# Kernel optimization log

Measured on AMD Instinct MI355X. Metric: run time of the kernel, lower is better.

Reference implementation:

```python
import jax, jax.numpy as jnp
import numpy as np

B, S, D_IN, D_HID, D_OUT, H = 2, 2048, 1024, 1024, 1024, 16
HD = D_HID // H  # head_dim = 64


def setup_inputs() -> dict:
    key = jax.random.key(0)
    ks = jax.random.split(key, 9)
    s_in = 1.0 / np.sqrt(D_IN)
    s_out = 1.0 / np.sqrt(D_OUT)
    return {
        "x": jax.random.normal(ks[0], (B, S, D_IN), dtype=jnp.float32),
        "Wq": jax.random.uniform(ks[1], (D_IN, D_HID), jnp.float32, -s_in, s_in),
        "bq": jax.random.uniform(ks[2], (D_HID,), jnp.float32, -s_in, s_in),
        "Wk": jax.random.uniform(ks[3], (D_IN, D_HID), jnp.float32, -s_in, s_in),
        "bk": jax.random.uniform(ks[4], (D_HID,), jnp.float32, -s_in, s_in),
        "Wv": jax.random.uniform(ks[5], (D_IN, D_OUT), jnp.float32, -s_in, s_in),
        "bv": jax.random.uniform(ks[6], (D_OUT,), jnp.float32, -s_in, s_in),
        "Wo": jax.random.uniform(ks[7], (D_OUT, D_OUT), jnp.float32, -s_out, s_out),
        "bo": jax.random.uniform(ks[8], (D_OUT,), jnp.float32, -s_out, s_out),
    }


def reference(x, Wq, bq, Wk, bk, Wv, bv, Wo, bo):
    b, s, _ = x.shape
    q = (x @ Wq + bq).reshape(b, s, H, HD)  # [B,S,H,HD]
    k = (x @ Wk + bk).reshape(b, s, H, HD)
    v = (x @ Wv + bv).reshape(b, s, H, HD)
    scores = jnp.einsum("bqhd,bkhd->bhqk", q, k) / jnp.sqrt(jnp.float32(HD))
    attn = jax.nn.softmax(scores, axis=-1)  # [B,H,S,S]
    ctx = jnp.einsum("bhqk,bkhd->bqhd", attn, v).reshape(b, s, D_HID)
    return ctx @ Wo + bo
```

## Files before the change

kernel.cpp:

```cpp
#include <hip/hip_runtime.h>
#include <stdint.h>

typedef __attribute__((ext_vector_type(8))) short short8v;
typedef __attribute__((ext_vector_type(4))) short short4v;
typedef __attribute__((ext_vector_type(4))) float float4v;
typedef __attribute__((ext_vector_type(4))) unsigned short ushort4v;
typedef __attribute__((ext_vector_type(4))) float floatvec4;
typedef __attribute__((ext_vector_type(2))) unsigned int uint2v;

#define DEVI __device__ __forceinline__

DEVI unsigned short f2bf(float f) {
    unsigned int u = __builtin_bit_cast(unsigned int, f);
    u += 0x7FFFu + ((u >> 16) & 1u);
    return (unsigned short)(u >> 16);
}

DEVI unsigned int pk2bf(float a, float b) {
#if defined(__has_builtin) && __has_builtin(__builtin_amdgcn_cvt_pk_bf16_f32)
    auto r = __builtin_amdgcn_cvt_pk_bf16_f32(a, b);
    unsigned int u;
    __builtin_memcpy(&u, &r, 4);
    return u;
#else
    return (unsigned int)f2bf(a) | ((unsigned int)f2bf(b) << 16);
#endif
}

DEVI float ex2(float x) {
#if defined(__has_builtin) && __has_builtin(__builtin_amdgcn_exp2f)
    return __builtin_amdgcn_exp2f(x);
#else
    return __builtin_exp2f(x);
#endif
}

typedef __attribute__((address_space(1))) void GV;
typedef __attribute__((address_space(3))) void LV;
DEVI void gl2lds16(const void* g, void* l) {
    __builtin_amdgcn_global_load_lds((GV*)g, (LV*)l, 16, 0, 0);
}

__global__ void prep_kernel(const float* __restrict__ x, unsigned short* __restrict__ xb,
                            const float* __restrict__ W0, const float* __restrict__ W1,
                            const float* __restrict__ W2, const float* __restrict__ W3,
                            unsigned short* __restrict__ D0, unsigned short* __restrict__ D1,
                            unsigned short* __restrict__ D2, unsigned short* __restrict__ D3) {
    const int bid = blockIdx.x, tid = threadIdx.x;
    if (bid < 4096) {
        const int i = (bid * 256 + tid) * 4;
        const floatvec4 v = *(const floatvec4*)&x[i];
        ushort4v o;
#pragma unroll
        for (int r = 0; r < 4; r++) o[r] = f2bf(v[r]);
        *(ushort4v*)&xb[i] = o;
        return;
    }
    __shared__ float t[32][33];
    const int tcode = bid - 4096;
    const int z = tcode >> 10, rem = tcode & 1023;
    const int by = rem >> 5, bx = rem & 31;
    const int tx = tid & 31, ty = tid >> 5;
    const float* W = (z == 0) ? W0 : (z == 1) ? W1 : (z == 2) ? W2 : W3;
    unsigned short* D = (z == 0) ? D0 : (z == 1) ? D1 : (z == 2) ? D2 : D3;
#pragma unroll
    for (int i = 0; i < 4; i++)
        t[ty + i * 8][tx] = W[(size_t)(by * 32 + ty + i * 8) * 1024 + bx * 32 + tx];
    __syncthreads();
#pragma unroll
    for (int i = 0; i < 4; i++)
        D[(size_t)(bx * 32 + ty + i * 8) * 1024 + by * 32 + tx] = f2bf(t[tx][ty + i * 8]);
}

__global__ __launch_bounds__(256, 3) void qkv_gemm(
    const unsigned short* __restrict__ X, const unsigned short* __restrict__ Wt,
    const float* __restrict__ bq, const float* __restrict__ bk, const float* __restrict__ bv,
    unsigned short* __restrict__ qb, unsigned short* __restrict__ kb,
    unsigned short* __restrict__ vtb)
{
    __shared__ __align__(16) unsigned short As[128 * 64];
    __shared__ __align__(16) unsigned short Bs[128 * 64];
    const int tid = threadIdx.x, lane = tid & 63, wv = tid >> 6;
    const int quad = lane >> 4, l16 = lane & 15;
    const int w = blockIdx.x >> 3;
    const int n0 = (blockIdx.x & 7) * 128;
    const int row0 = blockIdx.y * 128;
    const unsigned short* Wsel = Wt + (size_t)w * (1024 * 1024);

    const int srow = lane >> 3;
    const int qsc = ((lane & 7) ^ (lane >> 3 & 7)) * 8;
    const int fsw = l16 & 7;
    const int wm = (wv >> 1) * 64, wn = (wv & 1) * 64;

    float4v acc[4][4];
#pragma unroll
    for (int i = 0; i < 4; i++)
#pragma unroll
        for (int j = 0; j < 4; j++) acc[i][j] = (float4v){0.f, 0.f, 0.f, 0.f};

    for (int k0 = 0; k0 < 1024; k0 += 64) {
        __syncthreads();
#pragma unroll
        for (int i = 0; i < 4; i++) {
            const int c = wv * 4 + i;
            gl2lds16(X + (size_t)(row0 + c * 8 + srow) * 1024 + k0 + qsc, As + c * 512);
            gl2lds16(Wsel + (size_t)(n0 + c * 8 + srow) * 1024 + k0 + qsc, Bs + c * 512);
        }
        __syncthreads();
#pragma unroll
        for (int kc = 0; kc < 2; kc++) {
            const int sl = (((kc * 4 + quad) ^ fsw) * 8);
            short8v a[4], b[4];
#pragma unroll
            for (int mt = 0; mt < 4; mt++)
                a[mt] = *(const short8v*)&As[(wm + mt * 16 + l16) * 64 + sl];
#pragma unroll
            for (int nt = 0; nt < 4; nt++)
                b[nt] = *(const short8v*)&Bs[(wn + nt * 16 + l16) * 64 + sl];
#pragma unroll
            for (int mt = 0; mt < 4; mt++)
#pragma unroll
                for (int nt = 0; nt < 4; nt++)
                    acc[mt][nt] = __builtin_amdgcn_mfma_f32_16x16x32_bf16(a[mt], b[nt], acc[mt][nt], 0, 0, 0);
        }
    }

    const float* bias = (w == 0) ? bq : (w == 1) ? bk : bv;
    const float scl = (w == 0) ? 0.18033688011112042f : 1.0f;
#pragma unroll
    for (int nt = 0; nt < 4; nt++) {
        const int col = n0 + wn + nt * 16 + l16;
        const float bb = bias[col];
        const int h = col >> 6, hd = col & 63;
#pragma unroll
        for (int mt = 0; mt < 4; mt++) {
            const int tok0 = row0 + wm + mt * 16 + quad * 4;
            const int b_ = tok0 >> 11, s0 = tok0 & 2047;
            if (w == 2) {
                ushort4v pk;
#pragma unroll
                for (int r = 0; r < 4; r++) pk[r] = f2bf(acc[mt][nt][r] + bb);
                *(ushort4v*)&vtb[(((size_t)b_ * 16 + h) * 64 + hd) * 2048 + s0] = pk;
            } else {
                unsigned short* dst = (w == 0) ? qb : kb;
#pragma unroll
                for (int r = 0; r < 4; r++)
                    dst[(((size_t)b_ * 16 + h) * 2048 + (s0 + r)) * 64 + hd] =
                        f2bf((acc[mt][nt][r] + bb) * scl);
            }
        }
    }
}

__global__ __launch_bounds__(256, 2) void attn_kernel(
    const unsigned short* __restrict__ qb, const unsigned short* __restrict__ kb,
    const unsigned short* __restrict__ vtb, unsigned short* __restrict__ ctxb)
{
    __shared__ __align__(16) unsigned short Kt[128 * 64];
    __shared__ __align__(16) unsigned short Vt[64 * 128];
    __shared__ __align__(16) unsigned short Pb[4][32 * 128];
    const int tid = threadIdx.x, lane = tid & 63, wv = tid >> 6;
    const int quad = lane >> 4, l16 = lane & 15;
    const int bh = blockIdx.x, qt = blockIdx.y;
    const size_t boff = (size_t)bh * (2048 * 64);
    const unsigned short* qp = qb + boff;
    const unsigned short* kp = kb + boff;
    const unsigned short* vp = vtb + boff;
    const int q0 = qt * 128 + wv * 32;

    short8v qf[2][2];
#pragma unroll
    for (int nt = 0; nt < 2; nt++)
#pragma unroll
        for (int kc = 0; kc < 2; kc++)
            qf[nt][kc] = *(const short8v*)&qp[(size_t)(q0 + nt * 16 + l16) * 64 + kc * 32 + quad * 8];

    float4v accO[2][4];
#pragma unroll
    for (int nt = 0; nt < 2; nt++)
#pragma unroll
        for (int ht = 0; ht < 4; ht++) accO[nt][ht] = (float4v){0.f, 0.f, 0.f, 0.f};
    float lsum[2] = {0.f, 0.f};

    const int krow = lane >> 3;
    const int kg = (lane & 7) ^ (lane >> 3);
    const int vrow = lane >> 4;
    const int rsw = l16 & 7;

    const int ktb0 = l16 * 64 + ((quad ^ rsw) * 8);
    const int ktb1 = l16 * 64 + (((4 + quad) ^ rsw) * 8);
    const int vrb = l16 * 128 + ((quad ^ (l16 & 3)) * 8);
    const int l12e = (l16 & 12) * 8;
    const int prow = l16 * 128;

    for (int kt0 = 0; kt0 < 2048; kt0 += 128) {
        __syncthreads();
#pragma unroll
        for (int i = 0; i < 4; i++) {
            const int c = wv * 4 + i;
            gl2lds16(kp + (size_t)(kt0 + c * 8 + krow) * 64 + kg * 8, Kt + c * 512);
            const int vr = c * 4 + vrow;
            const int vg = (lane & 15) ^ (vr & 15);
            gl2lds16(vp + (size_t)vr * 2048 + kt0 + vg * 8, Vt + c * 512);
        }
        __syncthreads();

#pragma unroll
        for (int mt = 0; mt < 8; mt++) {
            const short8v a0 = *(const short8v*)&Kt[ktb0 + mt * 1024];
            const short8v a1 = *(const short8v*)&Kt[ktb1 + mt * 1024];
            const int pwo = prow + (((mt * 4 + quad) ^ l16) * 4);
#pragma unroll
            for (int nt = 0; nt < 2; nt++) {
                float4v z = (float4v){0.f, 0.f, 0.f, 0.f};
                z = __builtin_amdgcn_mfma_f32_16x16x32_bf16(a0, qf[nt][0], z, 0, 0, 0);
                z = __builtin_amdgcn_mfma_f32_16x16x32_bf16(a1, qf[nt][1], z, 0, 0, 0);
                const float p0 = ex2(z[0]), p1 = ex2(z[1]);
                const float p2 = ex2(z[2]), p3 = ex2(z[3]);
                lsum[nt] += (p0 + p1) + (p2 + p3);
                *(uint2v*)&Pb[wv][pwo + nt * 2048] = (uint2v){pk2bf(p0, p1), pk2bf(p2, p3)};
            }
        }
        asm volatile("s_waitcnt lgkmcnt(0)" ::: "memory");

#pragma unroll
        for (int kc = 0; kc < 4; kc++) {
            const int roff = (kc * 32) ^ l12e;
            short8v bvv[4];
#pragma unroll
            for (int ht = 0; ht < 4; ht++)
                bvv[ht] = *(const short8v*)&Vt[vrb + roff + ht * 2048];
            const int c0 = prow + (((kc * 8 + quad * 2) ^ l16) * 4);
            const int c1 = prow + (((kc * 8 + quad * 2 + 1) ^ l16) * 4);
#pragma unroll
            for (int nt = 0; nt < 2; nt++) {
                const short4v d0 = *(const short4v*)&Pb[wv][c0 + nt * 2048];
                const short4v d1 = *(const short4v*)&Pb[wv][c1 + nt * 2048];
                const short8v ap = __builtin_shufflevector(d0, d1, 0, 1, 2, 3, 4, 5, 6, 7);
#pragma unroll
                for (int ht = 0; ht < 4; ht++)
                    accO[nt][ht] = __builtin_amdgcn_mfma_f32_16x16x32_bf16(ap, bvv[ht], accO[nt][ht], 0, 0, 0);
            }
        }
    }

#pragma unroll
    for (int nt = 0; nt < 2; nt++) {
        lsum[nt] += __shfl_xor(lsum[nt], 16);
        lsum[nt] += __shfl_xor(lsum[nt], 32);
    }

    const int b_ = bh >> 4, h = bh & 15;
#pragma unroll
    for (int nt = 0; nt < 2; nt++)
#pragma unroll
        for (int r = 0; r < 4; r++) {
            const int s = q0 + nt * 16 + quad * 4 + r;
            const float inv = 1.0f / __shfl(lsum[nt], quad * 4 + r);
#pragma unroll
            for (int ht = 0; ht < 4; ht++) {
                const int hd = ht * 16 + l16;
                ctxb[((size_t)(b_ * 2048 + s)) * 1024 + h * 64 + hd] = f2bf(accO[nt][ht][r] * inv);
            }
        }
}

__global__ __launch_bounds__(256, 2) void out_gemm(
    const unsigned short* __restrict__ ctx, const unsigned short* __restrict__ Wot,
    const float* __restrict__ bo, float* __restrict__ out)
{
    __shared__ __align__(16) unsigned short As[128 * 64];
    __shared__ __align__(16) unsigned short Bs[64 * 64];
    const int tid = threadIdx.x, lane = tid & 63, wv = tid >> 6;
    const int quad = lane >> 4, l16 = lane & 15;
    const int n0 = blockIdx.x * 64;
    const int row0 = blockIdx.y * 128;

    const int srow = lane >> 3;
    const int qsc = ((lane & 7) ^ (lane >> 3 & 7)) * 8;
    const int fsw = l16 & 7;
    const int wm = (wv & 1) * 64, wn = (wv >> 1) * 32;

    float4v acc[4][2];
#pragma unroll
    for (int i = 0; i < 4; i++)
#pragma unroll
        for (int j = 0; j < 2; j++) acc[i][j] = (float4v){0.f, 0.f, 0.f, 0.f};

    for (int k0 = 0; k0 < 1024; k0 += 64) {
        __syncthreads();
#pragma unroll
        for (int i = 0; i < 6; i++) {
            const int c = wv * 6 + i;
            if (c < 16)
                gl2lds16(ctx + (size_t)(row0 + c * 8 + srow) * 1024 + k0 + qsc, As + c * 512);
            else
                gl2lds16(Wot + (size_t)(n0 + (c - 16) * 8 + srow) * 1024 + k0 + qsc,
                         Bs + (c - 16) * 512);
        }
        __syncthreads();
#pragma unroll
        for (int kc = 0; kc < 2; kc++) {
            const int sl = (((kc * 4 + quad) ^ fsw) * 8);
            short8v a[4], b[2];
#pragma unroll
            for (int mt = 0; mt < 4; mt++)
                a[mt] = *(const short8v*)&As[(wm + mt * 16 + l16) * 64 + sl];
#pragma unroll
            for (int nt = 0; nt < 2; nt++)
                b[nt] = *(const short8v*)&Bs[(wn + nt * 16 + l16) * 64 + sl];
#pragma unroll
            for (int mt = 0; mt < 4; mt++)
#pragma unroll
                for (int nt = 0; nt < 2; nt++)
                    acc[mt][nt] = __builtin_amdgcn_mfma_f32_16x16x32_bf16(a[mt], b[nt], acc[mt][nt], 0, 0, 0);
        }
    }

#pragma unroll
    for (int nt = 0; nt < 2; nt++) {
        const int col = n0 + wn + nt * 16 + l16;
        const float bb = bo[col];
#pragma unroll
        for (int mt = 0; mt < 4; mt++) {
            const int tok0 = row0 + wm + mt * 16 + quad * 4;
#pragma unroll
            for (int r = 0; r < 4; r++)
                out[(size_t)(tok0 + r) * 1024 + col] = acc[mt][nt][r] + bb;
        }
    }
}

extern "C" void kernel_launch(void* const* d_in, const int* in_sizes, int n_in,
                              void* d_out, int out_size, void* d_ws, size_t ws_size,
                              hipStream_t stream) {
    const float* x  = (const float*)d_in[0];
    const float* Wq = (const float*)d_in[1];
    const float* bq = (const float*)d_in[2];
    const float* Wk = (const float*)d_in[3];
    const float* bk = (const float*)d_in[4];
    const float* Wv = (const float*)d_in[5];
    const float* bv = (const float*)d_in[6];
    const float* Wo = (const float*)d_in[7];
    const float* bo = (const float*)d_in[8];
    float* out = (float*)d_out;

    char* ws = (char*)d_ws;
    unsigned short* xb   = (unsigned short*)(ws);
    unsigned short* qbuf = (unsigned short*)(ws + (8u << 20));
    unsigned short* kbuf = (unsigned short*)(ws + (16u << 20));
    unsigned short* vtb  = (unsigned short*)(ws + (24u << 20));
    unsigned short* wt   = (unsigned short*)(ws + (32u << 20));
    unsigned short* wot  = (unsigned short*)(ws + (38u << 20));

    prep_kernel<<<8192, 256, 0, stream>>>(x, xb, Wq, Wk, Wv, Wo,
                                          wt, wt + (1u << 20), wt + (2u << 20), wot);
    qkv_gemm<<<dim3(24, 32), 256, 0, stream>>>(xb, wt, bq, bk, bv, qbuf, kbuf, vtb);
    attn_kernel<<<dim3(32, 16), 256, 0, stream>>>(qbuf, kbuf, vtb, xb );
    out_gemm<<<dim3(16, 32), 256, 0, stream>>>(xb, wot, bo, out);
}
```

Measured before the change: 196.2 us.

## Double-buffer K/V tiles and pass P through registers via permlane swaps

The attention loop now double-buffers K and V tiles in LDS, issuing the next tile's global-to-LDS loads before computing the current one, so there is one barrier per iteration instead of two. The per-wave P staging buffer in LDS is removed. S=QK^T is computed in pairs of 16-key tiles, and the bf16 probabilities are rearranged into the MFMA A-operand layout with permlane32/permlane16 swaps instead of an LDS write and read-back. LDS use stays about the same, but if the permlane builtins are missing the fallback uses shuffles, and the lane/key ordering must match V's layout.

```diff
diff --git a/kernel.cpp b/kernel.cpp
--- a/kernel.cpp
+++ b/kernel.cpp
@@ -7,6 +7,7 @@
 typedef __attribute__((ext_vector_type(4))) unsigned short ushort4v;
 typedef __attribute__((ext_vector_type(4))) float floatvec4;
 typedef __attribute__((ext_vector_type(2))) unsigned int uint2v;
+typedef __attribute__((ext_vector_type(4))) unsigned int uint4v;
 
 #define DEVI __device__ __forceinline__
 
@@ -32,6 +33,25 @@
     return __builtin_amdgcn_exp2f(x);
 #else
     return __builtin_exp2f(x);
+#endif
+}
+
+DEVI uint2v pl32swap(unsigned int d, unsigned int s) {
+#if defined(__has_builtin) && __has_builtin(__builtin_amdgcn_permlane32_swap)
+    return __builtin_amdgcn_permlane32_swap(d, s, false, false);
+#else
+    const int hi = (int)(threadIdx.x & 32);
+    unsigned int dp = __shfl_xor(d, 32), sp = __shfl_xor(s, 32);
+    return (uint2v){hi ? sp : d, hi ? s : dp};
+#endif
+}
+DEVI uint2v pl16swap(unsigned int d, unsigned int s) {
+#if defined(__has_builtin) && __has_builtin(__builtin_amdgcn_permlane16_swap)
+    return __builtin_amdgcn_permlane16_swap(d, s, false, false);
+#else
+    const int lo = (int)(threadIdx.x & 16);
+    unsigned int dp = __shfl_xor(d, 16), sp = __shfl_xor(s, 16);
+    return (uint2v){lo ? sp : d, lo ? s : dp};
 #endif
 }
 
@@ -156,9 +176,8 @@
     const unsigned short* __restrict__ qb, const unsigned short* __restrict__ kb,
     const unsigned short* __restrict__ vtb, unsigned short* __restrict__ ctxb)
 {
-    __shared__ __align__(16) unsigned short Kt[128 * 64];
-    __shared__ __align__(16) unsigned short Vt[64 * 128];
-    __shared__ __align__(16) unsigned short Pb[4][32 * 128];
+    __shared__ __align__(16) unsigned short Kt[2 * 128 * 64];
+    __shared__ __align__(16) unsigned short Vt[2 * 64 * 128];
     const int tid = threadIdx.x, lane = tid & 63, wv = tid >> 6;
     const int quad = lane >> 4, l16 = lane & 15;
     const int bh = blockIdx.x, qt = blockIdx.y;
@@ -191,57 +210,67 @@
     const int ktb1 = l16 * 64 + (((4 + quad) ^ rsw) * 8);
     const int vrb = l16 * 128 + ((quad ^ (l16 & 3)) * 8);
     const int l12e = (l16 & 12) * 8;
-    const int prow = l16 * 128;
-
-    for (int kt0 = 0; kt0 < 2048; kt0 += 128) {
-        __syncthreads();
+
+    auto stage = [&](int kt0, int bn) {
+        unsigned short* Kd = Kt + bn * (128 * 64);
+        unsigned short* Vd = Vt + bn * (64 * 128);
 #pragma unroll
         for (int i = 0; i < 4; i++) {
             const int c = wv * 4 + i;
-            gl2lds16(kp + (size_t)(kt0 + c * 8 + krow) * 64 + kg * 8, Kt + c * 512);
+            gl2lds16(kp + (size_t)(kt0 + c * 8 + krow) * 64 + kg * 8, Kd + c * 512);
             const int vr = c * 4 + vrow;
             const int vg = (lane & 15) ^ (vr & 15);
-            gl2lds16(vp + (size_t)vr * 2048 + kt0 + vg * 8, Vt + c * 512);
-        }
-        __syncthreads();
-
-#pragma unroll
-        for (int mt = 0; mt < 8; mt++) {
-            const short8v a0 = *(const short8v*)&Kt[ktb0 + mt * 1024];
-            const short8v a1 = *(const short8v*)&Kt[ktb1 + mt * 1024];
-            const int pwo = prow + (((mt * 4 + quad) ^ l16) * 4);
-#pragma unroll
-            for (int nt = 0; nt < 2; nt++) {
-                float4v z = (float4v){0.f, 0.f, 0.f, 0.f};
-                z = __builtin_amdgcn_mfma_f32_16x16x32_bf16(a0, qf[nt][0], z, 0, 0, 0);
-                z = __builtin_amdgcn_mfma_f32_16x16x32_bf16(a1, qf[nt][1], z, 0, 0, 0);
-                const float p0 = ex2(z[0]), p1 = ex2(z[1]);
-                const float p2 = ex2(z[2]), p3 = ex2(z[3]);
-                lsum[nt] += (p0 + p1) + (p2 + p3);
-                *(uint2v*)&Pb[wv][pwo + nt * 2048] = (uint2v){pk2bf(p0, p1), pk2bf(p2, p3)};
-            }
-        }
-        asm volatile("s_waitcnt lgkmcnt(0)" ::: "memory");
+            gl2lds16(vp + (size_t)vr * 2048 + kt0 + vg * 8, Vd + c * 512);
+        }
+    };
+
+    stage(0, 0);
+    __syncthreads();
+
+    for (int t = 0; t < 16; ++t) {
+        if (t < 15) stage((t + 1) * 128, (t & 1) ^ 1);
+        const unsigned short* Kc = Kt + (t & 1) * (128 * 64);
+        const unsigned short* Vc = Vt + (t & 1) * (64 * 128);
 
 #pragma unroll
         for (int kc = 0; kc < 4; kc++) {
+            const int mt0 = 2 * kc, mt1 = 2 * kc + 1;
+            const short8v kA0 = *(const short8v*)&Kc[ktb0 + mt0 * 1024];
+            const short8v kA1 = *(const short8v*)&Kc[ktb1 + mt0 * 1024];
+            const short8v kB0 = *(const short8v*)&Kc[ktb0 + mt1 * 1024];
+            const short8v kB1 = *(const short8v*)&Kc[ktb1 + mt1 * 1024];
             const int roff = (kc * 32) ^ l12e;
             short8v bvv[4];
 #pragma unroll
             for (int ht = 0; ht < 4; ht++)
-                bvv[ht] = *(const short8v*)&Vt[vrb + roff + ht * 2048];
-            const int c0 = prow + (((kc * 8 + quad * 2) ^ l16) * 4);
-            const int c1 = prow + (((kc * 8 + quad * 2 + 1) ^ l16) * 4);
+                bvv[ht] = *(const short8v*)&Vc[vrb + roff + ht * 2048];
 #pragma unroll
             for (int nt = 0; nt < 2; nt++) {
-                const short4v d0 = *(const short4v*)&Pb[wv][c0 + nt * 2048];
-                const short4v d1 = *(const short4v*)&Pb[wv][c1 + nt * 2048];
-                const short8v ap = __builtin_shufflevector(d0, d1, 0, 1, 2, 3, 4, 5, 6, 7);
+                float4v za = (float4v){0.f, 0.f, 0.f, 0.f};
+                float4v zb = (float4v){0.f, 0.f, 0.f, 0.f};
+                za = __builtin_amdgcn_mfma_f32_16x16x32_bf16(kA0, qf[nt][0], za, 0, 0, 0);
+                za = __builtin_amdgcn_mfma_f32_16x16x32_bf16(kA1, qf[nt][1], za, 0, 0, 0);
+                zb = __builtin_amdgcn_mfma_f32_16x16x32_bf16(kB0, qf[nt][0], zb, 0, 0, 0);
+                zb = __builtin_amdgcn_mfma_f32_16x16x32_bf16(kB1, qf[nt][1], zb, 0, 0, 0);
+                const float pa0 = ex2(za[0]), pa1 = ex2(za[1]);
+                const float pa2 = ex2(za[2]), pa3 = ex2(za[3]);
+                const float pb0 = ex2(zb[0]), pb1 = ex2(zb[1]);
+                const float pb2 = ex2(zb[2]), pb3 = ex2(zb[3]);
+                lsum[nt] += ((pa0 + pa1) + (pa2 + pa3)) + ((pb0 + pb1) + (pb2 + pb3));
+                const unsigned int a0 = pk2bf(pa0, pa1), a1 = pk2bf(pa2, pa3);
+                const unsigned int b0 = pk2bf(pb0, pb1), b1 = pk2bf(pb2, pb3);
+                const uint2v s0 = pl32swap(a0, b0);
+                const uint2v s1 = pl32swap(a1, b1);
+                const uint2v t0 = pl16swap(s0.x, s0.y);
+                const uint2v t1 = pl16swap(s1.x, s1.y);
+                const uint4v fu = (uint4v){t0.x, t1.x, t0.y, t1.y};
+                const short8v ap = __builtin_bit_cast(short8v, fu);
 #pragma unroll
                 for (int ht = 0; ht < 4; ht++)
                     accO[nt][ht] = __builtin_amdgcn_mfma_f32_16x16x32_bf16(ap, bvv[ht], accO[nt][ht], 0, 0, 0);
             }
         }
+        __syncthreads();
     }
 
 #pragma unroll
```

New measurement: 196.2 us. Within noise of the previous version (-0.0%).

## Double-buffer K/V tiles in attention and split P buffer into halves

Applied to the files above, without the earlier changes.

Double-buffers the K and V shared-memory tiles so the global-to-LDS load of the next 128-key tile is issued before computing on the current one. This removes one of the two barriers per iteration and overlaps load latency with compute. The score/PV loop is split into two 64-key halves, so the per-wave P buffer shrinks to half size, offsetting the extra K/V LDS. The cost is more LDS overall, which may reduce occupancy, plus an extra lgkmcnt wait per half.

```diff
diff --git a/kernel.cpp b/kernel.cpp
--- a/kernel.cpp
+++ b/kernel.cpp
@@ -156,9 +156,9 @@
     const unsigned short* __restrict__ qb, const unsigned short* __restrict__ kb,
     const unsigned short* __restrict__ vtb, unsigned short* __restrict__ ctxb)
 {
-    __shared__ __align__(16) unsigned short Kt[128 * 64];
-    __shared__ __align__(16) unsigned short Vt[64 * 128];
-    __shared__ __align__(16) unsigned short Pb[4][32 * 128];
+    __shared__ __align__(16) unsigned short Kt[2 * 128 * 64];
+    __shared__ __align__(16) unsigned short Vt[2 * 64 * 128];
+    __shared__ __align__(16) unsigned short Pb[4][2 * 1024];
     const int tid = threadIdx.x, lane = tid & 63, wv = tid >> 6;
     const int quad = lane >> 4, l16 = lane & 15;
     const int bh = blockIdx.x, qt = blockIdx.y;
@@ -191,57 +191,72 @@
     const int ktb1 = l16 * 64 + (((4 + quad) ^ rsw) * 8);
     const int vrb = l16 * 128 + ((quad ^ (l16 & 3)) * 8);
     const int l12e = (l16 & 12) * 8;
-    const int prow = l16 * 128;
-
-    for (int kt0 = 0; kt0 < 2048; kt0 += 128) {
-        __syncthreads();
+    const int prow = l16 * 64;
+
+    auto stage = [&](int kt0, int bn) {
+        unsigned short* Kd = Kt + bn * (128 * 64);
+        unsigned short* Vd = Vt + bn * (64 * 128);
 #pragma unroll
         for (int i = 0; i < 4; i++) {
             const int c = wv * 4 + i;
-            gl2lds16(kp + (size_t)(kt0 + c * 8 + krow) * 64 + kg * 8, Kt + c * 512);
+            gl2lds16(kp + (size_t)(kt0 + c * 8 + krow) * 64 + kg * 8, Kd + c * 512);
             const int vr = c * 4 + vrow;
             const int vg = (lane & 15) ^ (vr & 15);
-            gl2lds16(vp + (size_t)vr * 2048 + kt0 + vg * 8, Vt + c * 512);
-        }
-        __syncthreads();
-
-#pragma unroll
-        for (int mt = 0; mt < 8; mt++) {
-            const short8v a0 = *(const short8v*)&Kt[ktb0 + mt * 1024];
-            const short8v a1 = *(const short8v*)&Kt[ktb1 + mt * 1024];
-            const int pwo = prow + (((mt * 4 + quad) ^ l16) * 4);
-#pragma unroll
-            for (int nt = 0; nt < 2; nt++) {
-                float4v z = (float4v){0.f, 0.f, 0.f, 0.f};
-                z = __builtin_amdgcn_mfma_f32_16x16x32_bf16(a0, qf[nt][0], z, 0, 0, 0);
-                z = __builtin_amdgcn_mfma_f32_16x16x32_bf16(a1, qf[nt][1], z, 0, 0, 0);
-                const float p0 = ex2(z[0]), p1 = ex2(z[1]);
-                const float p2 = ex2(z[2]), p3 = ex2(z[3]);
-                lsum[nt] += (p0 + p1) + (p2 + p3);
-                *(uint2v*)&Pb[wv][pwo + nt * 2048] = (uint2v){pk2bf(p0, p1), pk2bf(p2, p3)};
+            gl2lds16(vp + (size_t)vr * 2048 + kt0 + vg * 8, Vd + c * 512);
+        }
+    };
+
+    stage(0, 0);
+    __syncthreads();
+
+    for (int t = 0; t < 16; ++t) {
+        if (t < 15) stage((t + 1) * 128, (t & 1) ^ 1);
+        const unsigned short* Kc = Kt + (t & 1) * (128 * 64);
+        const unsigned short* Vc = Vt + (t & 1) * (64 * 128);
+
+#pragma unroll
+        for (int h = 0; h < 2; ++h) {
+#pragma unroll
+            for (int mt = 0; mt < 4; mt++) {
+                const int mtg = 4 * h + mt;
+                const short8v a0 = *(const short8v*)&Kc[ktb0 + mtg * 1024];
+                const short8v a1 = *(const short8v*)&Kc[ktb1 + mtg * 1024];
+                const int pwo = prow + (((mt * 4 + quad) ^ l16) * 4);
+#pragma unroll
+                for (int nt = 0; nt < 2; nt++) {
+                    float4v z = (float4v){0.f, 0.f, 0.f, 0.f};
+                    z = __builtin_amdgcn_mfma_f32_16x16x32_bf16(a0, qf[nt][0], z, 0, 0, 0);
+                    z = __builtin_amdgcn_mfma_f32_16x16x32_bf16(a1, qf[nt][1], z, 0, 0, 0);
+                    const float p0 = ex2(z[0]), p1 = ex2(z[1]);
+                    const float p2 = ex2(z[2]), p3 = ex2(z[3]);
+                    lsum[nt] += (p0 + p1) + (p2 + p3);
+                    *(uint2v*)&Pb[wv][pwo + nt * 1024] = (uint2v){pk2bf(p0, p1), pk2bf(p2, p3)};
+                }
             }
-        }
-        asm volatile("s_waitcnt lgkmcnt(0)" ::: "memory");
-
-#pragma unroll
-        for (int kc = 0; kc < 4; kc++) {
-            const int roff = (kc * 32) ^ l12e;
-            short8v bvv[4];
-#pragma unroll
-            for (int ht = 0; ht < 4; ht++)
-                bvv[ht] = *(const short8v*)&Vt[vrb + roff + ht * 2048];
-            const int c0 = prow + (((kc * 8 + quad * 2) ^ l16) * 4);
-            const int c1 = prow + (((kc * 8 + quad * 2 + 1) ^ l16) * 4);
-#pragma unroll
-            for (int nt = 0; nt < 2; nt++) {
-                const short4v d0 = *(const short4v*)&Pb[wv][c0 + nt * 2048];
-                const short4v d1 = *(const short4v*)&Pb[wv][c1 + nt * 2048];
-                const short8v ap = __builtin_shufflevector(d0, d1, 0, 1, 2, 3, 4, 5, 6, 7);
+            asm volatile("s_waitcnt lgkmcnt(0)" ::: "memory");
+
+#pragma unroll
+            for (int kcl = 0; kcl < 2; kcl++) {
+                const int kc = 2 * h + kcl;
+                const int roff = (kc * 32) ^ l12e;
+                short8v bvv[4];
 #pragma unroll
                 for (int ht = 0; ht < 4; ht++)
-                    accO[nt][ht] = __builtin_amdgcn_mfma_f32_16x16x32_bf16(ap, bvv[ht], accO[nt][ht], 0, 0, 0);
+                    bvv[ht] = *(const short8v*)&Vc[vrb + roff + ht * 2048];
+                const int c0 = prow + (((kcl * 8 + quad * 2) ^ l16) * 4);
+                const int c1 = prow + (((kcl * 8 + quad * 2 + 1) ^ l16) * 4);
+#pragma unroll
+                for (int nt = 0; nt < 2; nt++) {
+                    const short4v d0 = *(const short4v*)&Pb[wv][c0 + nt * 1024];
+                    const short4v d1 = *(const short4v*)&Pb[wv][c1 + nt * 1024];
+                    const short8v ap = __builtin_shufflevector(d0, d1, 0, 1, 2, 3, 4, 5, 6, 7);
+#pragma unroll
+                    for (int ht = 0; ht < 4; ht++)
+                        accO[nt][ht] = __builtin_amdgcn_mfma_f32_16x16x32_bf16(ap, bvv[ht], accO[nt][ht], 0, 0, 0);
+                }
             }
         }
+        __syncthreads();
     }
 
 #pragma unroll
```

Result: no change. 197.3 us (+0.5%).

## Enlarge QKV GEMM tiles to 256x256 with double-buffered LDS prefetch

Applied to the files above, without the earlier changes.

Rewrites the QKV projection GEMM to use 512-thread blocks that each compute a 256x256 output tile. The K loop is double-buffered in LDS, with global-to-LDS loads for the next K slice interleaved across four compute phases and MFMA sections raised in priority. The aim is to hide global load latency and get more reuse per tile. In exchange, the grid shrinks to 192 blocks, each thread holds more accumulator registers, and LDS use grows to 128KB per block, so occupancy and CU coverage drop. out_gemm's launch bounds are also raised to 3 blocks per CU.

```diff
diff --git a/kernel.cpp b/kernel.cpp
--- a/kernel.cpp
+++ b/kernel.cpp
@@ -72,56 +72,86 @@
         D[(size_t)(bx * 32 + ty + i * 8) * 1024 + by * 32 + tx] = f2bf(t[tx][ty + i * 8]);
 }
 
-__global__ __launch_bounds__(256, 3) void qkv_gemm(
+__global__ __launch_bounds__(512, 2) void qkv_gemm(
     const unsigned short* __restrict__ X, const unsigned short* __restrict__ Wt,
     const float* __restrict__ bq, const float* __restrict__ bk, const float* __restrict__ bv,
     unsigned short* __restrict__ qb, unsigned short* __restrict__ kb,
     unsigned short* __restrict__ vtb)
 {
-    __shared__ __align__(16) unsigned short As[128 * 64];
-    __shared__ __align__(16) unsigned short Bs[128 * 64];
+    __shared__ __align__(16) unsigned short As[2][256 * 64];
+    __shared__ __align__(16) unsigned short Bs[2][256 * 64];
     const int tid = threadIdx.x, lane = tid & 63, wv = tid >> 6;
     const int quad = lane >> 4, l16 = lane & 15;
-    const int w = blockIdx.x >> 3;
-    const int n0 = (blockIdx.x & 7) * 128;
-    const int row0 = blockIdx.y * 128;
+    const int w = blockIdx.x >> 2;
+    const int n0 = (blockIdx.x & 3) * 256;
+    const int row0 = blockIdx.y * 256;
     const unsigned short* Wsel = Wt + (size_t)w * (1024 * 1024);
 
     const int srow = lane >> 3;
-    const int qsc = ((lane & 7) ^ (lane >> 3 & 7)) * 8;
+    const int qsc = ((lane & 7) ^ srow) * 8;
     const int fsw = l16 & 7;
-    const int wm = (wv >> 1) * 64, wn = (wv & 1) * 64;
-
-    float4v acc[4][4];
-#pragma unroll
-    for (int i = 0; i < 4; i++)
+    const int wr = wv >> 2, wc = wv & 3;
+    const int wm = wr * 128, wn = wc * 64;
+
+    float4v acc[8][4];
+#pragma unroll
+    for (int i = 0; i < 8; i++)
 #pragma unroll
         for (int j = 0; j < 4; j++) acc[i][j] = (float4v){0.f, 0.f, 0.f, 0.f};
 
-    for (int k0 = 0; k0 < 1024; k0 += 64) {
-        __syncthreads();
-#pragma unroll
-        for (int i = 0; i < 4; i++) {
-            const int c = wv * 4 + i;
-            gl2lds16(X + (size_t)(row0 + c * 8 + srow) * 1024 + k0 + qsc, As + c * 512);
-            gl2lds16(Wsel + (size_t)(n0 + c * 8 + srow) * 1024 + k0 + qsc, Bs + c * 512);
-        }
-        __syncthreads();
-#pragma unroll
-        for (int kc = 0; kc < 2; kc++) {
-            const int sl = (((kc * 4 + quad) ^ fsw) * 8);
-            short8v a[4], b[4];
-#pragma unroll
-            for (int mt = 0; mt < 4; mt++)
-                a[mt] = *(const short8v*)&As[(wm + mt * 16 + l16) * 64 + sl];
-#pragma unroll
-            for (int nt = 0; nt < 4; nt++)
-                b[nt] = *(const short8v*)&Bs[(wn + nt * 16 + l16) * 64 + sl];
-#pragma unroll
-            for (int mt = 0; mt < 4; mt++)
-#pragma unroll
-                for (int nt = 0; nt < 4; nt++)
-                    acc[mt][nt] = __builtin_amdgcn_mfma_f32_16x16x32_bf16(a[mt], b[nt], acc[mt][nt], 0, 0, 0);
+    auto stageHalf = [&](int b, int k0, int op, int half) {
+#pragma unroll
+        for (int i = 0; i < 2; i++) {
+            const int c = half * 16 + wv * 2 + i;
+            const int r = c * 8 + srow;
+            if (op == 0)
+                gl2lds16(X + (size_t)(row0 + r) * 1024 + k0 + qsc, &As[b][c * 512]);
+            else
+                gl2lds16(Wsel + (size_t)(n0 + r) * 1024 + k0 + qsc, &Bs[b][c * 512]);
+        }
+    };
+
+    stageHalf(0, 0, 0, 0); stageHalf(0, 0, 0, 1);
+    stageHalf(0, 0, 1, 0); stageHalf(0, 0, 1, 1);
+    asm volatile("s_waitcnt vmcnt(0)" ::: "memory");
+    __builtin_amdgcn_s_barrier();
+
+    for (int t = 0; t < 16; ++t) {
+        const int b = t & 1;
+        const int nk0 = (t + 1) << 6;
+        const bool pf = (t < 15);
+#pragma unroll
+        for (int ph = 0; ph < 4; ++ph) {
+            const int qm = ph >> 1, qn = ph & 1;
+            short8v a[2][4], bw[2][2];
+#pragma unroll
+            for (int kc = 0; kc < 2; kc++) {
+                const int sl = ((kc * 4 + quad) ^ fsw) * 8;
+#pragma unroll
+                for (int i = 0; i < 4; i++)
+                    a[kc][i] = *(const short8v*)&As[b][(wm + (qm * 4 + i) * 16 + l16) * 64 + sl];
+#pragma unroll
+                for (int j = 0; j < 2; j++)
+                    bw[kc][j] = *(const short8v*)&Bs[b][(wn + (qn * 2 + j) * 16 + l16) * 64 + sl];
+            }
+            if (pf && ph < 2) {
+                stageHalf(b ^ 1, nk0, ph, 0);
+                stageHalf(b ^ 1, nk0, ph, 1);
+            }
+            asm volatile("s_waitcnt lgkmcnt(0)" ::: "memory");
+            __builtin_amdgcn_sched_barrier(0);
+            __builtin_amdgcn_s_setprio(1);
+#pragma unroll
+            for (int kc = 0; kc < 2; kc++)
+#pragma unroll
+                for (int i = 0; i < 4; i++)
+#pragma unroll
+                    for (int j = 0; j < 2; j++)
+                        acc[qm * 4 + i][qn * 2 + j] = __builtin_amdgcn_mfma_f32_16x16x32_bf16(
+                            a[kc][i], bw[kc][j], acc[qm * 4 + i][qn * 2 + j], 0, 0, 0);
+            __builtin_amdgcn_s_setprio(0);
+            if (ph == 3) asm volatile("s_waitcnt vmcnt(0)" ::: "memory");
+            __builtin_amdgcn_s_barrier();
         }
     }
 
@@ -133,7 +163,7 @@
         const float bb = bias[col];
         const int h = col >> 6, hd = col & 63;
 #pragma unroll
-        for (int mt = 0; mt < 4; mt++) {
+        for (int mt = 0; mt < 8; mt++) {
             const int tok0 = row0 + wm + mt * 16 + quad * 4;
             const int b_ = tok0 >> 11, s0 = tok0 & 2047;
             if (w == 2) {
@@ -265,7 +295,7 @@
         }
 }
 
-__global__ __launch_bounds__(256, 2) void out_gemm(
+__global__ __launch_bounds__(256, 3) void out_gemm(
     const unsigned short* __restrict__ ctx, const unsigned short* __restrict__ Wot,
     const float* __restrict__ bo, float* __restrict__ out)
 {
@@ -355,7 +385,7 @@
 
     prep_kernel<<<8192, 256, 0, stream>>>(x, xb, Wq, Wk, Wv, Wo,
                                           wt, wt + (1u << 20), wt + (2u << 20), wot);
-    qkv_gemm<<<dim3(24, 32), 256, 0, stream>>>(xb, wt, bq, bk, bv, qbuf, kbuf, vtb);
+    qkv_gemm<<<dim3(12, 16), 512, 0, stream>>>(xb, wt, bq, bk, bv, qbuf, kbuf, vtb);
     attn_kernel<<<dim3(32, 16), 256, 0, stream>>>(qbuf, kbuf, vtb, xb );
     out_gemm<<<dim3(16, 32), 256, 0, stream>>>(xb, wot, bo, out);
 }
```

New measurement: 205.4 us. +4.7%, slower.
